# Optimization experiments

Measured on AMD Instinct MI355X. Metric: run time of the kernel, lower is better.

## Reference

```python
import jax, jax.numpy as jnp
import numpy as np

K2 = 4.0 / 3.0; K4 = 4.10451; K5 = 19.08857; K6 = 254.5553148552
KN = 7.5; WF = 6.0; GA = 3.0; GC = 2.0
BOHR = 0.5291772105638411; HARTREE = 27.211386024367243
C2BOHR = 1.0 / BOHR; C2EV = 0.5 * HARTREE
N_ATOMS = 50000; N_NEIGH = 48; ZMAX = 87; NREF = 7; NFREQ = 23; KCN = 7


def _sp_inv(x):
    # softplus_inverse
    return jnp.float32(np.log(np.expm1(x)))


def setup_inputs() -> dict:
    key = jax.random.key(0)
    ks = jax.random.split(key, 24)
    P = N_ATOMS * N_NEIGH
    u = lambda k, shp, lo, hi: jax.random.uniform(k, shp, jnp.float32, lo, hi)
    Z = jax.random.randint(ks[0], (N_ATOMS,), 0, ZMAX)
    idx_i = jnp.repeat(jnp.arange(N_ATOMS), N_NEIGH)  # center index per pair
    idx_j = jax.random.randint(ks[1], (P,), 0, N_ATOMS)
    r_ij = u(ks[2], (P,), 1.5, 6.0)  # Angstrom
    qa = 0.05 * jax.random.normal(ks[3], (N_ATOMS,), jnp.float32)
    return dict(
        Z=Z, idx_i=idx_i, idx_j=idx_j, r_ij=r_ij, qa=qa,
        s6_raw=_sp_inv(1.0), s8_raw=_sp_inv(1.61679827),
        a1_raw=_sp_inv(0.44959224), a2_raw=_sp_inv(3.35743605),
        scaleq_raw=_sp_inv(1.0),
        refsys=jax.random.randint(ks[4], (ZMAX, NREF), 0, ZMAX),
        zeff=u(ks[5], (ZMAX,), 1.0, 10.0),
        refh=u(ks[6], (ZMAX, NREF), 0.0, 0.3),
        sscale=u(ks[7], (ZMAX,), 0.5, 1.5),
        secaiw=u(ks[8], (ZMAX, NFREQ), 0.0, 1.0),
        gam=u(ks[9], (ZMAX,), 0.05, 0.5),
        ascale=u(ks[10], (ZMAX, NREF), 0.5, 1.5),
        alphaiw=u(ks[11], (ZMAX, NREF, NFREQ), 0.0, 5.0),
        hcount=u(ks[12], (ZMAX, NREF), 0.0, 2.0),
        casimir_polder_weights=u(ks[13], (NFREQ,), 0.0, 0.5),
        rcov=u(ks[14], (ZMAX,), 0.6, 2.5),
        en=u(ks[15], (ZMAX,), 0.5, 4.0),
        ncount_mask=(u(ks[16], (ZMAX, NREF, KCN), 0.0, 1.0) < 0.6).astype(jnp.float32),
        ncount_weight=u(ks[17], (ZMAX, NREF, KCN), 0.5, 2.0),
        cn=u(ks[18], (ZMAX, NREF, KCN), 0.0, 6.0),
        fixgweights=(lambda g: g / jnp.sum(g, -1, keepdims=True))(u(ks[19], (ZMAX, NREF), 0.1, 1.0)),
        refq=u(ks[20], (ZMAX, NREF), -0.2, 0.2),
        sqrt_r4r2=u(ks[21], (ZMAX,), 1.0, 4.0),
    )


def compute_refc6(scaleq, refsys, zeff, refh, sscale, secaiw, gam, ascale, alphaiw, hcount, cpw):
    iz = zeff[refsys]                                   # [Z, nref]
    qref = iz
    qmod = iz + refh * scaleq
    qmod_ = jnp.where(qmod > 1e-8, qmod, 1.0)
    zeta = jnp.where(qmod > 1e-8,
                     jnp.exp(GA * (1.0 - jnp.exp(gam[refsys] * GC * (1.0 - qref / qmod_)))),
                     np.exp(GA).astype(np.float32))
    asec = sscale[refsys][..., None] * secaiw[refsys] * zeta[..., None]  # [Z,nref,nfreq]
    alpha = jnp.maximum(ascale[..., None] * (alphaiw - hcount[..., None] * asec), 0.0)
    return (3.0 / np.pi) * jnp.einsum('iax,jbx,x->ijab', alpha, alpha, cpw)  # [Z,Z,nref,nref]


def reference(Z, idx_i, idx_j, r_ij, qa, s6_raw, s8_raw, a1_raw, a2_raw, scaleq_raw,
              refsys, zeff, refh, sscale, secaiw, gam, ascale, alphaiw, hcount,
              casimir_polder_weights, rcov, en, ncount_mask, ncount_weight, cn,
              fixgweights, refq, sqrt_r4r2):
    n_atoms = qa.shape[0]
    scaleq = jax.nn.softplus(scaleq_raw)
    # refc6 is computed under no_grad in the original module
    refc6 = jax.lax.stop_gradient(compute_refc6(scaleq, refsys, zeff, refh, sscale,
                                                secaiw, gam, ascale, alphaiw, hcount,
                                                casimir_polder_weights))
    r = r_ij * C2BOHR
    Zi = Z[idx_i]; Zj = Z[idx_j]
    # coordination-number contribution per pair, scattered to centers
    rco = K2 * (rcov[Zi] + rcov[Zj])
    den = K4 * jnp.exp(-(jnp.abs(en[Zi] - en[Zj]) + K5) ** 2 / K6)
    tmp = den * 0.5 * (1.0 + jax.lax.erf(-KN * (r - rco) / rco))
    covcn = jax.ops.segment_sum(tmp, idx_i, num_segments=n_atoms)
    # gaussian reference-CN weights [n_atoms, nref]
    gweights = jnp.sum(ncount_mask[Z] * jnp.exp(-WF * ncount_weight[Z] * (covcn[:, None, None] - cn[Z]) ** 2), -1)
    norm = jnp.sum(gweights, -1, keepdims=True)
    gweights = jnp.where(norm > 1e-8, gweights / jnp.where(norm > 1e-8, norm, 1.0), fixgweights[Z])
    # charge scaling zeta [n_atoms, nref]
    iz = zeff[Z][:, None]
    qref = iz + refq[Z] * scaleq
    qmod = iz + qa[:, None]
    qmod_ = jnp.where(qmod > 1e-8, qmod, 1.0)
    zeta = jnp.where(qmod > 1e-8,
                     jnp.exp(GA * (1.0 - jnp.exp(gam[Z][:, None] * GC * (1.0 - qref / qmod_)))),
                     np.exp(GA).astype(np.float32)) * gweights
    zetai = zeta[idx_i]; zetaj = zeta[idx_j]            # [P, nref]
    refc6ij = refc6[Zi, Zj]                             # [P, nref, nref]
    c6ij = jnp.einsum('pab,pa,pb->p', refc6ij, zetai, zetaj)
    r4r2ij = np.float32(np.sqrt(3.0)) * sqrt_r4r2[Zi] * sqrt_r4r2[Zj]
    a1 = jax.nn.softplus(a1_raw); a2 = jax.nn.softplus(a2_raw)
    r0 = a1 * r4r2ij + a2
    oor6 = 1.0 / (r ** 6 + r0 ** 6)
    oor8 = 1.0 / (r ** 8 + r0 ** 8)
    s6 = jax.nn.softplus(s6_raw); s8 = jax.nn.softplus(s8_raw)
    edisp = -c6ij * (s6 * oor6 + s8 * r4r2ij ** 2 * oor8) * C2EV
    eatom = jax.ops.segment_sum(edisp, idx_i, num_segments=n_atoms)
    zeros = jnp.zeros((n_atoms,), r_ij.dtype)  # compute_atomic_quantities=False
    return (eatom, zeros, zeros)
```

## Files before the change

### kernel.cpp

```cpp
#include <hip/hip_runtime.h>
#include <math.h>

#define NATOMS 50000
#define NNEIGH 48
#define ZMAXV 87
#define NREFV 7
#define NFREQV 23
#define KCNV 7
#define XPAD 24
#define ATOMS_PER_BLOCK 4
#define PAIR_BLOCK (ATOMS_PER_BLOCK * NNEIGH)

#define C2BOHR 1.8897261258369282f
#define C2EV 13.605693012183622f
#define K2C 1.33333333333333333f
#define K4C 4.10451f
#define K5C 19.08857f
#define K6INV (1.0f / 254.5553148552f)
#define KNC 7.5f
#define EXP_GA 20.085536923187668f
#define SQRT3 1.7320508075688772f

__device__ __forceinline__ float sp(float x) { return log1pf(expf(x)); }

__global__ __launch_bounds__(256) void k_setup(
    const int* __restrict__ refsys, const float* __restrict__ zeff,
    const float* __restrict__ refh, const float* __restrict__ sscale,
    const float* __restrict__ secaiw, const float* __restrict__ gam,
    const float* __restrict__ ascale, const float* __restrict__ alphaiw,
    const float* __restrict__ hcount,
    const float* __restrict__ s6r, const float* __restrict__ s8r,
    const float* __restrict__ a1r, const float* __restrict__ a2r,
    const float* __restrict__ sqr,
    float* __restrict__ scal_out, float* __restrict__ alpha_out,
    float* __restrict__ zero_out)
{
    int e = blockIdx.x * 256 + threadIdx.x;
    if (e == 0) {
        scal_out[0] = sp(s6r[0]);
        scal_out[1] = sp(s8r[0]);
        scal_out[2] = sp(a1r[0]);
        scal_out[3] = sp(a2r[0]);
    }
    if (e < 2 * NATOMS) zero_out[e] = 0.0f;
    if (e < ZMAXV * NREFV * XPAD) {
        int x = e % XPAD;
        int za = e / XPAD;
        float v = 0.0f;
        if (x < NFREQV) {
            float scaleq = sp(sqr[0]);
            int rs = refsys[za];
            float iz = zeff[rs];
            float qmod = iz + refh[za] * scaleq;
            float zeta = (qmod > 1e-8f)
                ? __expf(3.0f * (1.0f - __expf(gam[rs] * 2.0f * (1.0f - iz / qmod))))
                : EXP_GA;
            float asec = sscale[rs] * secaiw[rs * NFREQV + x] * zeta;
            v = fmaxf(ascale[za] * (alphaiw[za * NFREQV + x] - hcount[za] * asec), 0.0f);
        }
        alpha_out[e] = v;
    }
}

__global__ __launch_bounds__(PAIR_BLOCK) void k_atoms(
    const int* __restrict__ Z, const int* __restrict__ idx_j,
    const float* __restrict__ r_ij, const float* __restrict__ qa,
    const float* __restrict__ sqr, const float* __restrict__ zeff,
    const float* __restrict__ gam, const float* __restrict__ rcov,
    const float* __restrict__ en, const float* __restrict__ nmask,
    const float* __restrict__ nweight, const float* __restrict__ cn,
    const float* __restrict__ fixg, const float* __restrict__ refq,
    const float* __restrict__ cpw, const float* __restrict__ alpha_tab,
    float* __restrict__ A_out)
{
    __shared__ float sh[PAIR_BLOCK];
    __shared__ float covcn[ATOMS_PER_BLOCK];
    __shared__ float gwl[ATOMS_PER_BLOCK][NREFV];
    __shared__ float ztl[ATOMS_PER_BLOCK][NREFV];
    const int t = threadIdx.x;
    const int a0 = blockIdx.x * ATOMS_PER_BLOCK;

    {
        int p = blockIdx.x * PAIR_BLOCK + t;
        int atom = a0 + (t / NNEIGH);
        int zi = Z[atom];
        int j = idx_j[p];
        int zj = Z[j];
        float r = r_ij[p] * C2BOHR;
        float rco = K2C * (rcov[zi] + rcov[zj]);
        float d = fabsf(en[zi] - en[zj]) + K5C;
        float den = K4C * __expf(-d * d * K6INV);
        float tmp = den * 0.5f * (1.0f + erff(-KNC * (r - rco) / rco));
        sh[t] = tmp;
    }
    __syncthreads();
    if (t < ATOMS_PER_BLOCK) {
        float s = 0.0f;
        for (int k = 0; k < NNEIGH; k++) s += sh[t * NNEIGH + k];
        covcn[t] = s;
    }
    __syncthreads();

    if (t < ATOMS_PER_BLOCK * NREFV) {
        int al = t / NREFV, a = t % NREFV;
        int zl = Z[a0 + al];
        float cc = covcn[al];
        const float* mB = nmask + (zl * NREFV + a) * KCNV;
        const float* wB = nweight + (zl * NREFV + a) * KCNV;
        const float* cB = cn + (zl * NREFV + a) * KCNV;
        float g = 0.0f;
        for (int k = 0; k < KCNV; k++) {
            float dc = cc - cB[k];
            g += mB[k] * __expf(-6.0f * wB[k] * dc * dc);
        }
        gwl[al][a] = g;
    }
    __syncthreads();

    if (t < ATOMS_PER_BLOCK * NREFV) {
        int al = t / NREFV, a = t % NREFV;
        int zl = Z[a0 + al];
        float norm = 0.0f;
        for (int b = 0; b < NREFV; b++) norm += gwl[al][b];
        float w = (norm > 1e-8f) ? (gwl[al][a] / norm) : fixg[zl * NREFV + a];
        float scaleq = sp(sqr[0]);
        float iz = zeff[zl];
        float qref = iz + refq[zl * NREFV + a] * scaleq;
        float qmod = iz + qa[a0 + al];
        float zeta = (qmod > 1e-8f)
            ? __expf(3.0f * (1.0f - __expf(gam[zl] * 2.0f * (1.0f - qref / qmod))))
            : EXP_GA;
        ztl[al][a] = zeta * w;
    }
    __syncthreads();

    if (t < ATOMS_PER_BLOCK * XPAD) {
        int al = t / XPAD, x = t % XPAD;
        float v = 0.0f;
        if (x < NFREQV) {
            int zl = Z[a0 + al];
            float s = 0.0f;
            #pragma unroll
            for (int a = 0; a < NREFV; a++)
                s += ztl[al][a] * alpha_tab[(zl * NREFV + a) * XPAD + x];
            v = s * sqrtf(cpw[x] * 0.9549296585513721f);
        }
        A_out[a0 * XPAD + t] = v;
    }
}

__global__ __launch_bounds__(PAIR_BLOCK) void k_pairs(
    const int* __restrict__ Z, const int* __restrict__ idx_j,
    const float* __restrict__ r_ij, const float* __restrict__ scal,
    const float* __restrict__ sr4r2, const float* __restrict__ A,
    float* __restrict__ eatom)
{
    __shared__ float sh[PAIR_BLOCK];
    __shared__ float Ai[ATOMS_PER_BLOCK * XPAD];
    const int t = threadIdx.x;
    const int a0 = blockIdx.x * ATOMS_PER_BLOCK;

    if (t < ATOMS_PER_BLOCK * XPAD) Ai[t] = A[a0 * XPAD + t];
    __syncthreads();

    const float s6 = scal[0], s8 = scal[1], a1 = scal[2], a2 = scal[3];

    int p = blockIdx.x * PAIR_BLOCK + t;
    int al = t / NNEIGH;
    int atom = a0 + al;
    int j = idx_j[p];
    int zi = Z[atom], zj = Z[j];
    float r = r_ij[p] * C2BOHR;

    const float4* Aj4 = (const float4*)(A + (size_t)j * XPAD);
    const float* Aib = Ai + al * XPAD;
    float c6 = 0.0f;
    #pragma unroll
    for (int q = 0; q < XPAD / 4; q++) {
        float4 v = Aj4[q];
        c6 += v.x * Aib[4 * q + 0] + v.y * Aib[4 * q + 1] +
              v.z * Aib[4 * q + 2] + v.w * Aib[4 * q + 3];
    }

    float r4r2 = SQRT3 * sr4r2[zi] * sr4r2[zj];
    float r0 = a1 * r4r2 + a2;
    float r2 = r * r, r4 = r2 * r2, r6 = r4 * r2, r8 = r4 * r4;
    float p2 = r0 * r0, p4 = p2 * p2, p6 = p4 * p2, p8 = p4 * p4;
    float oor6 = 1.0f / (r6 + p6);
    float oor8 = 1.0f / (r8 + p8);
    float e = -c6 * (s6 * oor6 + s8 * r4r2 * r4r2 * oor8) * C2EV;

    sh[t] = e;
    __syncthreads();
    if (t < ATOMS_PER_BLOCK) {
        float s = 0.0f;
        for (int k = 0; k < NNEIGH; k++) s += sh[t * NNEIGH + k];
        eatom[a0 + t] = s;
    }
}

extern "C" void kernel_launch(void* const* d_in, const int* in_sizes, int n_in,
                              void* d_out, int out_size, void* d_ws, size_t ws_size,
                              hipStream_t stream)
{
    const int*   Z       = (const int*)  d_in[0];
    const int*   idx_j   = (const int*)  d_in[2];
    const float* r_ij    = (const float*)d_in[3];
    const float* qa      = (const float*)d_in[4];
    const float* s6r     = (const float*)d_in[5];
    const float* s8r     = (const float*)d_in[6];
    const float* a1r     = (const float*)d_in[7];
    const float* a2r     = (const float*)d_in[8];
    const float* sqraw   = (const float*)d_in[9];
    const int*   refsys  = (const int*)  d_in[10];
    const float* zeff    = (const float*)d_in[11];
    const float* refh    = (const float*)d_in[12];
    const float* sscale  = (const float*)d_in[13];
    const float* secaiw  = (const float*)d_in[14];
    const float* gam     = (const float*)d_in[15];
    const float* ascale  = (const float*)d_in[16];
    const float* alphaiw = (const float*)d_in[17];
    const float* hcount  = (const float*)d_in[18];
    const float* cpw     = (const float*)d_in[19];
    const float* rcov    = (const float*)d_in[20];
    const float* en      = (const float*)d_in[21];
    const float* nmask   = (const float*)d_in[22];
    const float* nweight = (const float*)d_in[23];
    const float* cn      = (const float*)d_in[24];
    const float* fixg    = (const float*)d_in[25];
    const float* refq    = (const float*)d_in[26];
    const float* sr4r2   = (const float*)d_in[27];

    float* ws    = (float*)d_ws;
    float* scal  = ws;
    float* alpha = ws + 16;
    float* Avec  = ws + 16 + ZMAXV * NREFV * XPAD;

    float* eatom = (float*)d_out;
    float* zeros = eatom + NATOMS;

    k_setup<<<391, 256, 0, stream>>>(refsys, zeff, refh, sscale, secaiw, gam,
                                     ascale, alphaiw, hcount, s6r, s8r, a1r, a2r,
                                     sqraw, scal, alpha, zeros);
    k_atoms<<<NATOMS / ATOMS_PER_BLOCK, PAIR_BLOCK, 0, stream>>>(
        Z, idx_j, r_ij, qa, sqraw, zeff, gam, rcov, en,
        nmask, nweight, cn, fixg, refq, cpw, alpha, Avec);
    k_pairs<<<NATOMS / ATOMS_PER_BLOCK, PAIR_BLOCK, 0, stream>>>(
        Z, idx_j, r_ij, scal, sr4r2, Avec, eatom);
}
```

Baseline: 196.3 us.

## Store per-atom A vectors in fp16 with packed r4r2 factor, precompute per-atom rcov/en

The per-atom Casimir-Polder vector is now stored in half precision, padded to 32 entries, with the square-root r4r2 factor packed into slot 23. Each random neighbor gather in the pair kernel then reads 48 bytes instead of 96 plus separate Z and sr4r2 lookups. k_setup also precomputes a per-atom (rcov, en) float2 so the coordination-number pass avoids the double indirection through Z. Storing A in fp16 lowers the precision of C6 and of the r4r2 factor, which risks tolerance failures.

```diff
diff --git a/kernel.cpp b/kernel.cpp
--- a/kernel.cpp
+++ b/kernel.cpp
@@ -1,4 +1,5 @@
 #include <hip/hip_runtime.h>
+#include <hip/hip_fp16.h>
 #include <math.h>
 
 #define NATOMS 50000
@@ -8,6 +9,7 @@
 #define NFREQV 23
 #define KCNV 7
 #define XPAD 24
+#define XPADH 32
 #define ATOMS_PER_BLOCK 4
 #define PAIR_BLOCK (ATOMS_PER_BLOCK * NNEIGH)
 
@@ -19,21 +21,22 @@
 #define K6INV (1.0f / 254.5553148552f)
 #define KNC 7.5f
 #define EXP_GA 20.085536923187668f
-#define SQRT3 1.7320508075688772f
+#define QRT3 1.3160740129524924f
 
 __device__ __forceinline__ float sp(float x) { return log1pf(expf(x)); }
 
 __global__ __launch_bounds__(256) void k_setup(
-    const int* __restrict__ refsys, const float* __restrict__ zeff,
-    const float* __restrict__ refh, const float* __restrict__ sscale,
-    const float* __restrict__ secaiw, const float* __restrict__ gam,
-    const float* __restrict__ ascale, const float* __restrict__ alphaiw,
-    const float* __restrict__ hcount,
+    const int* __restrict__ Z, const int* __restrict__ refsys,
+    const float* __restrict__ zeff, const float* __restrict__ refh,
+    const float* __restrict__ sscale, const float* __restrict__ secaiw,
+    const float* __restrict__ gam, const float* __restrict__ ascale,
+    const float* __restrict__ alphaiw, const float* __restrict__ hcount,
+    const float* __restrict__ rcov, const float* __restrict__ en,
     const float* __restrict__ s6r, const float* __restrict__ s8r,
     const float* __restrict__ a1r, const float* __restrict__ a2r,
     const float* __restrict__ sqr,
     float* __restrict__ scal_out, float* __restrict__ alpha_out,
-    float* __restrict__ zero_out)
+    float2* __restrict__ re2_out, float* __restrict__ zero_out)
 {
     int e = blockIdx.x * 256 + threadIdx.x;
     if (e == 0) {
@@ -43,6 +46,10 @@
         scal_out[3] = sp(a2r[0]);
     }
     if (e < 2 * NATOMS) zero_out[e] = 0.0f;
+    if (e < NATOMS) {
+        int z = Z[e];
+        re2_out[e] = make_float2(rcov[z], en[z]);
+    }
     if (e < ZMAXV * NREFV * XPAD) {
         int x = e % XPAD;
         int za = e / XPAD;
@@ -66,12 +73,12 @@
     const int* __restrict__ Z, const int* __restrict__ idx_j,
     const float* __restrict__ r_ij, const float* __restrict__ qa,
     const float* __restrict__ sqr, const float* __restrict__ zeff,
-    const float* __restrict__ gam, const float* __restrict__ rcov,
-    const float* __restrict__ en, const float* __restrict__ nmask,
-    const float* __restrict__ nweight, const float* __restrict__ cn,
-    const float* __restrict__ fixg, const float* __restrict__ refq,
-    const float* __restrict__ cpw, const float* __restrict__ alpha_tab,
-    float* __restrict__ A_out)
+    const float* __restrict__ gam, const float2* __restrict__ re2,
+    const float* __restrict__ nmask, const float* __restrict__ nweight,
+    const float* __restrict__ cn, const float* __restrict__ fixg,
+    const float* __restrict__ refq, const float* __restrict__ cpw,
+    const float* __restrict__ alpha_tab, const float* __restrict__ sr4r2,
+    __half* __restrict__ A_out)
 {
     __shared__ float sh[PAIR_BLOCK];
     __shared__ float covcn[ATOMS_PER_BLOCK];
@@ -83,15 +90,13 @@
     {
         int p = blockIdx.x * PAIR_BLOCK + t;
         int atom = a0 + (t / NNEIGH);
-        int zi = Z[atom];
-        int j = idx_j[p];
-        int zj = Z[j];
+        float2 rei = re2[atom];
+        float2 rej = re2[idx_j[p]];
         float r = r_ij[p] * C2BOHR;
-        float rco = K2C * (rcov[zi] + rcov[zj]);
-        float d = fabsf(en[zi] - en[zj]) + K5C;
+        float rco = K2C * (rei.x + rej.x);
+        float d = fabsf(rei.y - rej.y) + K5C;
         float den = K4C * __expf(-d * d * K6INV);
-        float tmp = den * 0.5f * (1.0f + erff(-KNC * (r - rco) / rco));
-        sh[t] = tmp;
+        sh[t] = den * 0.5f * (1.0f + erff(-KNC * (r - rco) / rco));
     }
     __syncthreads();
     if (t < ATOMS_PER_BLOCK) {
@@ -134,55 +139,72 @@
     }
     __syncthreads();
 
-    if (t < ATOMS_PER_BLOCK * XPAD) {
-        int al = t / XPAD, x = t % XPAD;
+    if (t < ATOMS_PER_BLOCK * XPADH) {
+        int al = t / XPADH, x = t % XPADH;
+        int zl = Z[a0 + al];
         float v = 0.0f;
         if (x < NFREQV) {
-            int zl = Z[a0 + al];
             float s = 0.0f;
             #pragma unroll
             for (int a = 0; a < NREFV; a++)
                 s += ztl[al][a] * alpha_tab[(zl * NREFV + a) * XPAD + x];
             v = s * sqrtf(cpw[x] * 0.9549296585513721f);
-        }
-        A_out[a0 * XPAD + t] = v;
+        } else if (x == NFREQV) {
+            v = QRT3 * sr4r2[zl];
+        }
+        A_out[(size_t)a0 * XPADH + t] = __float2half(v);
     }
 }
 
 __global__ __launch_bounds__(PAIR_BLOCK) void k_pairs(
-    const int* __restrict__ Z, const int* __restrict__ idx_j,
-    const float* __restrict__ r_ij, const float* __restrict__ scal,
-    const float* __restrict__ sr4r2, const float* __restrict__ A,
+    const int* __restrict__ idx_j, const float* __restrict__ r_ij,
+    const float* __restrict__ scal, const __half* __restrict__ Ah,
     float* __restrict__ eatom)
 {
     __shared__ float sh[PAIR_BLOCK];
-    __shared__ float Ai[ATOMS_PER_BLOCK * XPAD];
+    __shared__ float Ai[ATOMS_PER_BLOCK][NFREQV];
+    __shared__ float Asi[ATOMS_PER_BLOCK];
     const int t = threadIdx.x;
     const int a0 = blockIdx.x * ATOMS_PER_BLOCK;
 
-    if (t < ATOMS_PER_BLOCK * XPAD) Ai[t] = A[a0 * XPAD + t];
+    if (t < ATOMS_PER_BLOCK * XPADH) {
+        int al = t >> 5, x = t & 31;
+        float v = __half2float(Ah[(size_t)a0 * XPADH + t]);
+        if (x < NFREQV) Ai[al][x] = v;
+        else if (x == NFREQV) Asi[al] = v;
+    }
     __syncthreads();
 
     const float s6 = scal[0], s8 = scal[1], a1 = scal[2], a2 = scal[3];
 
     int p = blockIdx.x * PAIR_BLOCK + t;
     int al = t / NNEIGH;
-    int atom = a0 + al;
     int j = idx_j[p];
-    int zi = Z[atom], zj = Z[j];
     float r = r_ij[p] * C2BOHR;
 
-    const float4* Aj4 = (const float4*)(A + (size_t)j * XPAD);
-    const float* Aib = Ai + al * XPAD;
+    const float4* Aj4 = (const float4*)(Ah + (size_t)j * XPADH);
+    float4 w0 = Aj4[0], w1 = Aj4[1], w2 = Aj4[2];
+    float a[24];
+    {
+        const __half2* h0 = (const __half2*)&w0;
+        const __half2* h1 = (const __half2*)&w1;
+        const __half2* h2 = (const __half2*)&w2;
+        #pragma unroll
+        for (int k = 0; k < 4; k++) {
+            float2 f0 = __half22float2(h0[k]);
+            float2 f1 = __half22float2(h1[k]);
+            float2 f2 = __half22float2(h2[k]);
+            a[2 * k]      = f0.x; a[2 * k + 1]      = f0.y;
+            a[8 + 2 * k]  = f1.x; a[8 + 2 * k + 1]  = f1.y;
+            a[16 + 2 * k] = f2.x; a[16 + 2 * k + 1] = f2.y;
+        }
+    }
     float c6 = 0.0f;
     #pragma unroll
-    for (int q = 0; q < XPAD / 4; q++) {
-        float4 v = Aj4[q];
-        c6 += v.x * Aib[4 * q + 0] + v.y * Aib[4 * q + 1] +
-              v.z * Aib[4 * q + 2] + v.w * Aib[4 * q + 3];
-    }
-
-    float r4r2 = SQRT3 * sr4r2[zi] * sr4r2[zj];
+    for (int x = 0; x < NFREQV; x++) c6 += a[x] * Ai[al][x];
+    float sj = a[NFREQV];
+
+    float r4r2 = Asi[al] * sj;
     float r0 = a1 * r4r2 + a2;
     float r2 = r * r, r4 = r2 * r2, r6 = r4 * r2, r8 = r4 * r4;
     float p2 = r0 * r0, p4 = p2 * p2, p6 = p4 * p2, p8 = p4 * p4;
@@ -234,17 +256,19 @@
     float* ws    = (float*)d_ws;
     float* scal  = ws;
     float* alpha = ws + 16;
-    float* Avec  = ws + 16 + ZMAXV * NREFV * XPAD;
+    float2* re2  = (float2*)(ws + 16 + ZMAXV * NREFV * XPAD);
+    __half* Ah   = (__half*)(ws + 16 + ZMAXV * NREFV * XPAD + 2 * NATOMS);
 
     float* eatom = (float*)d_out;
     float* zeros = eatom + NATOMS;
 
-    k_setup<<<391, 256, 0, stream>>>(refsys, zeff, refh, sscale, secaiw, gam,
-                                     ascale, alphaiw, hcount, s6r, s8r, a1r, a2r,
-                                     sqraw, scal, alpha, zeros);
+    k_setup<<<391, 256, 0, stream>>>(Z, refsys, zeff, refh, sscale, secaiw, gam,
+                                     ascale, alphaiw, hcount, rcov, en,
+                                     s6r, s8r, a1r, a2r, sqraw,
+                                     scal, alpha, re2, zeros);
     k_atoms<<<NATOMS / ATOMS_PER_BLOCK, PAIR_BLOCK, 0, stream>>>(
-        Z, idx_j, r_ij, qa, sqraw, zeff, gam, rcov, en,
-        nmask, nweight, cn, fixg, refq, cpw, alpha, Avec);
+        Z, idx_j, r_ij, qa, sqraw, zeff, gam, re2,
+        nmask, nweight, cn, fixg, refq, cpw, alpha, sr4r2, Ah);
     k_pairs<<<NATOMS / ATOMS_PER_BLOCK, PAIR_BLOCK, 0, stream>>>(
-        Z, idx_j, r_ij, scal, sr4r2, Avec, eatom);
-}
+        idx_j, r_ij, scal, Ah, eatom);
+}
```

Result: faster. 177.7 us (-9.5%).
